# Optimization experiments

Hardware: AMD Instinct MI355X
Metric: run time of the kernel (lower is better)

## Reference

```python
import jax, jax.numpy as jnp
import numpy as np

N, D, E, L = 50000, 128, 800000, 3


def setup_inputs() -> dict:
    key = jax.random.key(0)
    ks = jax.random.split(key, 4)
    scale = 1.0 / np.sqrt(D)
    x = jax.random.normal(ks[0], (N, D), dtype=jnp.float32)
    edge_index = jax.random.randint(ks[1], (2, E), 0, N, dtype=jnp.int64)
    W1 = jax.random.normal(ks[2], (L, D, D), dtype=jnp.float32) * scale
    W2 = jax.random.normal(ks[3], (L, D, D), dtype=jnp.float32) * scale
    b1 = jnp.zeros((L, D), dtype=jnp.float32)
    b2 = jnp.zeros((L, D), dtype=jnp.float32)
    return {"x": x, "edge_index": edge_index, "W1": W1, "b1": b1, "W2": W2, "b2": b2}


def reference(x, edge_index, W1, b1, W2, b2):
    # GIN: for each conv, agg_i = (1+eps)*x_i + sum_{(j->i)} x_j  (eps=0),
    # then h = nn(agg) with nn = Linear->ReLU->Linear, then outer ReLU.
    src = edge_index[0]
    dst = edge_index[1]
    n = x.shape[0]
    for l in range(W1.shape[0]):
        agg = x + jax.ops.segment_sum(x[src], dst, num_segments=n)  # [N, D]
        h = jnp.maximum(agg @ W1[l] + b1[l], 0.0)                   # inner ReLU
        x = jnp.maximum(h @ W2[l] + b2[l], 0.0)                     # outer ReLU
    return x
```

## Files before the change

### kernel.cpp

```cpp
#include <hip/hip_runtime.h>
#include <cstdint>


constexpr int N = 50000;
constexpr int D = 128;
constexpr int E = 800000;
constexpr int L = 3;
constexpr int WROW = 136;
constexpr int PSH = 9;
constexpr int PN = 1 << PSH;
constexpr int K = (N + PN - 1) >> PSH;
constexpr int ABLK = 2048;
constexpr int NAB = (E + ABLK - 1) / ABLK;

typedef _Float16 f16;
typedef _Float16 f16x8 __attribute__((ext_vector_type(8)));
typedef float f32x4 __attribute__((ext_vector_type(4)));

__device__ __forceinline__ bool ei_is64(const int* ei) {
  return (ei[1] == 0) && (ei[3] == 0) && (ei[5] == 0);
}
__device__ __forceinline__ int ei_src(const int* ei, int e, bool is64) {
  return is64 ? ei[2 * (size_t)e] : ei[e];
}
__device__ __forceinline__ int ei_dst(const int* ei, int e, bool is64) {
  return is64 ? ei[2 * ((size_t)E + e)] : ei[(size_t)E + e];
}

__global__ __launch_bounds__(256) void k_init(const float* __restrict__ x0,
                                              const int* __restrict__ ei,
                                              const float* __restrict__ W1,
                                              const float* __restrict__ W2,
                                              f16* __restrict__ Wt,
                                              f16* __restrict__ xh,
                                              int2* __restrict__ srcdst,
                                              int* __restrict__ gcnt) {
  __shared__ int hist[K];
  const int bid = blockIdx.x;
  if (bid < 384) {
    int i = bid * 256 + threadIdx.x;
    int m = i >> 14;
    int c = (i >> 7) & 127;
    int k = i & 127;
    const float* src = (m < L) ? (W1 + (size_t)m * D * D)
                               : (W2 + (size_t)(m - L) * D * D);
    Wt[i] = (f16)src[(size_t)k * D + c];
  } else if (bid < 384 + 3125) {
    int i = (bid - 384) * 256 + threadIdx.x;
    float4 v0 = *(const float4*)(x0 + (size_t)i * 8);
    float4 v1 = *(const float4*)(x0 + (size_t)i * 8 + 4);
    f16x8 o = {(f16)v0.x, (f16)v0.y, (f16)v0.z, (f16)v0.w,
               (f16)v1.x, (f16)v1.y, (f16)v1.z, (f16)v1.w};
    *(f16x8*)(xh + (size_t)i * 8) = o;
  } else {
    const int b = bid - (384 + 3125);
    for (int i = threadIdx.x; i < K; i += 256) hist[i] = 0;
    __syncthreads();
    const int base = b * ABLK;
    const int nHere = min(ABLK, E - base);
    bool is64 = ei_is64(ei);
#pragma unroll
    for (int r = 0; r < ABLK / 256; ++r) {
      int idx = r * 256 + threadIdx.x;
      if (idx < nHere) {
        int e = base + idx;
        int s = ei_src(ei, e, is64);
        int d = ei_dst(ei, e, is64);
        srcdst[e] = make_int2(s, d);
        atomicAdd(&hist[d >> PSH], 1);
      }
    }
    __syncthreads();
    for (int i = threadIdx.x; i < K; i += 256) gcnt[i * NAB + b] = hist[i];
  }
}

__global__ __launch_bounds__(256) void k_gbase(const int* __restrict__ gcnt,
                                               int* __restrict__ gbase,
                                               int* __restrict__ psize) {
  __shared__ int s[256];
  __shared__ int carry;
  const int p = blockIdx.x;
  const int tid = threadIdx.x;
  if (tid == 0) carry = 0;
  __syncthreads();
  for (int chunk = 0; chunk < 2; ++chunk) {
    int i = chunk * 256 + tid;
    int v = (i < NAB) ? gcnt[p * NAB + i] : 0;
    s[tid] = v;
    __syncthreads();
#pragma unroll
    for (int o = 1; o < 256; o <<= 1) {
      int t = (tid >= o) ? s[tid - o] : 0;
      __syncthreads();
      s[tid] += t;
      __syncthreads();
    }
    int excl = s[tid] - v + carry;
    if (i < NAB) gbase[p * NAB + i] = excl;
    __syncthreads();
    if (tid == 255) carry = carry + s[255];
    __syncthreads();
  }
  if (tid == 0) psize[p] = carry;
}

__global__ __launch_bounds__(256) void k_pscan(const int* __restrict__ psize,
                                               int* __restrict__ pbase,
                                               int* __restrict__ off) {
  __shared__ int s[256];
  const int tid = threadIdx.x;
  int v = (tid < K) ? psize[tid] : 0;
  s[tid] = v;
  __syncthreads();
#pragma unroll
  for (int o = 1; o < 256; o <<= 1) {
    int t = (tid >= o) ? s[tid - o] : 0;
    __syncthreads();
    s[tid] += t;
    __syncthreads();
  }
  if (tid < K) pbase[tid] = s[tid] - v;
  if (tid == 0) { pbase[K] = E; off[N] = E; }
}

__global__ __launch_bounds__(256) void k_scat(const int2* __restrict__ srcdst,
                                              const int* __restrict__ gbase,
                                              const int* __restrict__ pbase,
                                              int2* __restrict__ part) {
  __shared__ int rankc[K];
  const int b = blockIdx.x;
  const int tid = threadIdx.x;
  for (int i = tid; i < K; i += 256) rankc[i] = 0;
  __syncthreads();
  const int base = b * ABLK;
  const int nHere = min(ABLK, E - base);
#pragma unroll
  for (int r = 0; r < ABLK / 256; ++r) {
    int idx = r * 256 + tid;
    if (idx < nHere) {
      int2 sd = srcdst[base + idx];
      int p = sd.y >> PSH;
      int lr = atomicAdd(&rankc[p], 1);
      part[pbase[p] + gbase[p * NAB + b] + lr] = sd;
    }
  }
}

__global__ __launch_bounds__(256) void k_fin(const int2* __restrict__ part,
                                             const int* __restrict__ pbase,
                                             int* __restrict__ off,
                                             int* __restrict__ ssrc) {
  __shared__ int hist[PN];
  __shared__ int bbase[PN];
  __shared__ int rc[PN];
  __shared__ int s[256];
  __shared__ int carry;
  const int p = blockIdx.x;
  const int tid = threadIdx.x;
  const int lo = p << PSH;
  const int nn = min(PN, N - lo);
  const int ebeg = pbase[p], eend = pbase[p + 1];
  for (int i = tid; i < PN; i += 256) { hist[i] = 0; rc[i] = 0; }
  if (tid == 0) carry = 0;
  __syncthreads();
  for (int e = ebeg + tid; e < eend; e += 256)
    atomicAdd(&hist[part[e].y - lo], 1);
  __syncthreads();
  for (int chunk = 0; chunk < PN / 256; ++chunk) {
    int i = chunk * 256 + tid;
    int v = hist[i];
    s[tid] = v;
    __syncthreads();
#pragma unroll
    for (int o = 1; o < 256; o <<= 1) {
      int t = (tid >= o) ? s[tid - o] : 0;
      __syncthreads();
      s[tid] += t;
      __syncthreads();
    }
    bbase[i] = s[tid] - v + carry;
    __syncthreads();
    if (tid == 255) carry = carry + s[255];
    __syncthreads();
  }
  for (int i = tid; i < nn; i += 256) off[lo + i] = ebeg + bbase[i];
  __syncthreads();
  for (int e = ebeg + tid; e < eend; e += 256) {
    int2 sd = part[e];
    int b = sd.y - lo;
    int r = atomicAdd(&rc[b], 1);
    ssrc[ebeg + bbase[b] + r] = sd.x;
  }
}

__global__ __launch_bounds__(256) void k_gather_f16(const f16* __restrict__ x,
                                                    const int* __restrict__ off,
                                                    const int* __restrict__ ssrc,
                                                    f16* __restrict__ agg) {
  int n = blockIdx.x * 16 + (threadIdx.x >> 4);
  if (n >= N) return;
  const int d0 = (threadIdx.x & 15) << 3;
  f16x8 v = *(const f16x8*)(x + (size_t)n * D + d0);
  float acc[8];
#pragma unroll
  for (int j = 0; j < 8; ++j) acc[j] = (float)v[j];
  const int beg = off[n], end = off[n + 1];
  int p = beg;
  for (; p + 8 <= end; p += 8) {
    f16x8 u[8];
#pragma unroll
    for (int q = 0; q < 8; ++q) {
      int s = ssrc[p + q];
      u[q] = *(const f16x8*)(x + (size_t)s * D + d0);
    }
#pragma unroll
    for (int q = 0; q < 8; ++q)
#pragma unroll
      for (int j = 0; j < 8; ++j) acc[j] += (float)u[q][j];
  }
  if (p + 4 <= end) {
    f16x8 u[4];
#pragma unroll
    for (int q = 0; q < 4; ++q) {
      int s = ssrc[p + q];
      u[q] = *(const f16x8*)(x + (size_t)s * D + d0);
    }
#pragma unroll
    for (int q = 0; q < 4; ++q)
#pragma unroll
      for (int j = 0; j < 8; ++j) acc[j] += (float)u[q][j];
    p += 4;
  }
  for (; p < end; ++p) {
    int s = ssrc[p];
    f16x8 u = *(const f16x8*)(x + (size_t)s * D + d0);
#pragma unroll
    for (int j = 0; j < 8; ++j) acc[j] += (float)u[j];
  }
  f16x8 o;
#pragma unroll
  for (int j = 0; j < 8; ++j) o[j] = (f16)acc[j];
  *(f16x8*)(agg + (size_t)n * D + d0) = o;
}

__global__ __launch_bounds__(512) void k_gemm_fused(const f16* __restrict__ A,
                                                    const f16* __restrict__ Wt1,
                                                    const f16* __restrict__ Wt2,
                                                    const float* __restrict__ b1,
                                                    const float* __restrict__ b2,
                                                    f16* __restrict__ Ch,
                                                    float* __restrict__ Cf) {
  __shared__ f16 Ws[2][128 * WROW];
  {
    const f16x8* g1 = (const f16x8*)Wt1;
    const f16x8* g2 = (const f16x8*)Wt2;
    for (int i = threadIdx.x; i < 2048; i += 512) {
      int c = i >> 4;
      int k8 = (i & 15) << 3;
      *(f16x8*)&Ws[0][c * WROW + k8] = g1[i];
      *(f16x8*)&Ws[1][c * WROW + k8] = g2[i];
    }
  }

  const int w = threadIdx.x >> 6;
  const int l = threadIdx.x & 63;
  const int l15 = l & 15;
  const int g = l >> 4;
  const int r0 = blockIdx.x * 128 + w * 16;

  const int arow = min(r0 + l15, N - 1);
  const f16* Arow = A + (size_t)arow * D;
  f16x8 a[4];
#pragma unroll
  for (int t = 0; t < 4; ++t)
    a[t] = *(const f16x8*)(Arow + t * 32 + g * 8);

  float bc1[8], bc2[8];
#pragma unroll
  for (int c = 0; c < 8; ++c) {
    bc1[c] = b1[c * 16 + l15];
    bc2[c] = b2[c * 16 + l15];
  }
  __syncthreads();

  f32x4 acc[8];
#pragma unroll
  for (int c = 0; c < 8; ++c) acc[c] = (f32x4){0.f, 0.f, 0.f, 0.f};
#pragma unroll
  for (int t = 0; t < 4; ++t) {
#pragma unroll
    for (int c = 0; c < 8; ++c) {
      f16x8 b = *(const f16x8*)&Ws[0][(c * 16 + l15) * WROW + t * 32 + g * 8];
      acc[c] = __builtin_amdgcn_mfma_f32_16x16x32_f16(a[t], b, acc[c], 0, 0, 0);
    }
  }
  __syncthreads();

  f16* hbuf = &Ws[0][0];
#pragma unroll
  for (int r = 0; r < 4; ++r) {
    int hr = w * 16 + g * 4 + r;
#pragma unroll
    for (int c = 0; c < 8; ++c) {
      float vv = fmaxf(acc[c][r] + bc1[c], 0.0f);
      hbuf[hr * WROW + c * 16 + l15] = (f16)vv;
    }
  }
  __syncthreads();

  f16x8 a2[4];
#pragma unroll
  for (int t = 0; t < 4; ++t)
    a2[t] = *(const f16x8*)&hbuf[(w * 16 + l15) * WROW + t * 32 + g * 8];

#pragma unroll
  for (int c = 0; c < 8; ++c) acc[c] = (f32x4){0.f, 0.f, 0.f, 0.f};
#pragma unroll
  for (int t = 0; t < 4; ++t) {
#pragma unroll
    for (int c = 0; c < 8; ++c) {
      f16x8 b = *(const f16x8*)&Ws[1][(c * 16 + l15) * WROW + t * 32 + g * 8];
      acc[c] = __builtin_amdgcn_mfma_f32_16x16x32_f16(a2[t], b, acc[c], 0, 0, 0);
    }
  }

#pragma unroll
  for (int r = 0; r < 4; ++r) {
    int rr = r0 + g * 4 + r;
    if (rr < N) {
#pragma unroll
      for (int c = 0; c < 8; ++c) {
        int col = c * 16 + l15;
        float vv = fmaxf(acc[c][r] + bc2[c], 0.0f);
        if (Cf) Cf[(size_t)rr * D + col] = vv;
        else    Ch[(size_t)rr * D + col] = (f16)vv;
      }
    }
  }
}

extern "C" void kernel_launch(void* const* d_in, const int* in_sizes, int n_in,
                              void* d_out, int out_size, void* d_ws, size_t ws_size,
                              hipStream_t stream) {
  const float* x0 = (const float*)d_in[0];
  const int* ei   = (const int*)d_in[1];
  const float* W1 = (const float*)d_in[2];
  const float* b1 = (const float*)d_in[3];
  const float* W2 = (const float*)d_in[4];
  const float* b2 = (const float*)d_in[5];
  float* out = (float*)d_out;

  f16* xh      = (f16*)d_ws;
  f16* aggh    = xh + (size_t)N * D;
  f16* Wt      = aggh + (size_t)N * D;
  int2* srcdst = (int2*)(Wt + (size_t)2 * L * D * D);
  int2* part   = srcdst + E;
  int* gcnt    = (int*)(part + E);
  int* gbase   = gcnt + (size_t)K * NAB;
  int* psize   = gbase + (size_t)K * NAB;
  int* pbase   = psize + K;
  int* off     = pbase + (K + 1);
  int* ssrc    = off + (N + 1);

  const dim3 blk(256);

  k_init<<<384 + 3125 + NAB, blk, 0, stream>>>(x0, ei, W1, W2, Wt, xh, srcdst,
                                               gcnt);
  k_gbase<<<K, blk, 0, stream>>>(gcnt, gbase, psize);
  k_pscan<<<1, blk, 0, stream>>>(psize, pbase, off);
  k_scat<<<NAB, blk, 0, stream>>>(srcdst, gbase, pbase, part);
  k_fin<<<K, blk, 0, stream>>>(part, pbase, off, ssrc);

  const int gemm_blocks = (N + 127) / 128;
  const int gather_blocks = N / 16;

  for (int l = 0; l < L; ++l) {
    k_gather_f16<<<gather_blocks, blk, 0, stream>>>(xh, off, ssrc, aggh);
    k_gemm_fused<<<gemm_blocks, dim3(512), 0, stream>>>(
        aggh, Wt + (size_t)l * D * D, Wt + (size_t)(L + l) * D * D,
        b1 + (size_t)l * D, b2 + (size_t)l * D, xh,
        (l == L - 1) ? out : nullptr);
  }
}
```

Baseline: 182.4 us.

## Pad CSR neighbor lists to multiples of eight with a zero dummy row

```diff
diff --git a/kernel.cpp b/kernel.cpp
--- a/kernel.cpp
+++ b/kernel.cpp
@@ -10,6 +10,7 @@
 constexpr int PSH = 9;
 constexpr int PN = 1 << PSH;
 constexpr int K = (N + PN - 1) >> PSH;
+constexpr int SLACK = 7 * PN;
 constexpr int ABLK = 2048;
 constexpr int NAB = (E + ABLK - 1) / ABLK;
 
@@ -52,7 +53,7 @@
     f16x8 o = {(f16)v0.x, (f16)v0.y, (f16)v0.z, (f16)v0.w,
                (f16)v1.x, (f16)v1.y, (f16)v1.z, (f16)v1.w};
     *(f16x8*)(xh + (size_t)i * 8) = o;
-  } else {
+  } else if (bid < 384 + 3125 + NAB) {
     const int b = bid - (384 + 3125);
     for (int i = threadIdx.x; i < K; i += 256) hist[i] = 0;
     __syncthreads();
@@ -72,6 +73,9 @@
     }
     __syncthreads();
     for (int i = threadIdx.x; i < K; i += 256) gcnt[i * NAB + b] = hist[i];
+  } else {
+    if (threadIdx.x < 16)
+      *(f16x8*)(xh + (size_t)N * D + threadIdx.x * 8) = (f16x8){};
   }
 }
 
@@ -105,34 +109,32 @@
   if (tid == 0) psize[p] = carry;
 }
 
-__global__ __launch_bounds__(256) void k_pscan(const int* __restrict__ psize,
-                                               int* __restrict__ pbase,
-                                               int* __restrict__ off) {
-  __shared__ int s[256];
+__device__ __forceinline__ void pscan_inblock(const int* __restrict__ psize,
+                                              int* __restrict__ pb) {
   const int tid = threadIdx.x;
-  int v = (tid < K) ? psize[tid] : 0;
-  s[tid] = v;
-  __syncthreads();
-#pragma unroll
-  for (int o = 1; o < 256; o <<= 1) {
-    int t = (tid >= o) ? s[tid - o] : 0;
-    __syncthreads();
-    s[tid] += t;
-    __syncthreads();
-  }
-  if (tid < K) pbase[tid] = s[tid] - v;
-  if (tid == 0) { pbase[K] = E; off[N] = E; }
+  if (tid < K) pb[tid] = psize[tid];
+  __syncthreads();
+  if (tid == 0) {
+    int r = 0;
+    for (int i = 0; i < K; ++i) {
+      int v = pb[i];
+      pb[i] = r;
+      r += v;
+    }
+  }
+  __syncthreads();
 }
 
 __global__ __launch_bounds__(256) void k_scat(const int2* __restrict__ srcdst,
                                               const int* __restrict__ gbase,
-                                              const int* __restrict__ pbase,
+                                              const int* __restrict__ psize,
                                               int2* __restrict__ part) {
   __shared__ int rankc[K];
+  __shared__ int pb[K];
   const int b = blockIdx.x;
   const int tid = threadIdx.x;
   for (int i = tid; i < K; i += 256) rankc[i] = 0;
-  __syncthreads();
+  pscan_inblock(psize, pb);
   const int base = b * ABLK;
   const int nHere = min(ABLK, E - base);
 #pragma unroll
@@ -142,34 +144,37 @@
       int2 sd = srcdst[base + idx];
       int p = sd.y >> PSH;
       int lr = atomicAdd(&rankc[p], 1);
-      part[pbase[p] + gbase[p * NAB + b] + lr] = sd;
+      part[pb[p] + gbase[p * NAB + b] + lr] = sd;
     }
   }
 }
 
 __global__ __launch_bounds__(256) void k_fin(const int2* __restrict__ part,
-                                             const int* __restrict__ pbase,
+                                             const int* __restrict__ psize,
                                              int* __restrict__ off,
+                                             int* __restrict__ offend,
                                              int* __restrict__ ssrc) {
   __shared__ int hist[PN];
   __shared__ int bbase[PN];
   __shared__ int rc[PN];
   __shared__ int s[256];
+  __shared__ int pb[K];
   __shared__ int carry;
   const int p = blockIdx.x;
   const int tid = threadIdx.x;
   const int lo = p << PSH;
   const int nn = min(PN, N - lo);
-  const int ebeg = pbase[p], eend = pbase[p + 1];
   for (int i = tid; i < PN; i += 256) { hist[i] = 0; rc[i] = 0; }
   if (tid == 0) carry = 0;
-  __syncthreads();
+  pscan_inblock(psize, pb);
+  const int ebeg = pb[p], eend = pb[p] + psize[p];
+  const int padbase = pb[p] + p * SLACK;
   for (int e = ebeg + tid; e < eend; e += 256)
     atomicAdd(&hist[part[e].y - lo], 1);
   __syncthreads();
   for (int chunk = 0; chunk < PN / 256; ++chunk) {
     int i = chunk * 256 + tid;
-    int v = hist[i];
+    int v = (hist[i] + 7) & ~7;
     s[tid] = v;
     __syncthreads();
 #pragma unroll
@@ -184,30 +189,36 @@
     if (tid == 255) carry = carry + s[255];
     __syncthreads();
   }
-  for (int i = tid; i < nn; i += 256) off[lo + i] = ebeg + bbase[i];
+  for (int i = tid; i < nn; i += 256) {
+    int st = padbase + bbase[i];
+    int deg = hist[i];
+    int pd = (deg + 7) & ~7;
+    off[lo + i] = st;
+    offend[lo + i] = st + pd;
+    for (int j = deg; j < pd; ++j) ssrc[st + j] = N;
+  }
   __syncthreads();
   for (int e = ebeg + tid; e < eend; e += 256) {
     int2 sd = part[e];
     int b = sd.y - lo;
     int r = atomicAdd(&rc[b], 1);
-    ssrc[ebeg + bbase[b] + r] = sd.x;
+    ssrc[padbase + bbase[b] + r] = sd.x;
   }
 }
 
 __global__ __launch_bounds__(256) void k_gather_f16(const f16* __restrict__ x,
                                                     const int* __restrict__ off,
+                                                    const int* __restrict__ offend,
                                                     const int* __restrict__ ssrc,
                                                     f16* __restrict__ agg) {
   int n = blockIdx.x * 16 + (threadIdx.x >> 4);
-  if (n >= N) return;
   const int d0 = (threadIdx.x & 15) << 3;
   f16x8 v = *(const f16x8*)(x + (size_t)n * D + d0);
   float acc[8];
 #pragma unroll
   for (int j = 0; j < 8; ++j) acc[j] = (float)v[j];
-  const int beg = off[n], end = off[n + 1];
-  int p = beg;
-  for (; p + 8 <= end; p += 8) {
+  const int e = offend[n];
+  for (int p = off[n]; p < e; p += 8) {
     f16x8 u[8];
 #pragma unroll
     for (int q = 0; q < 8; ++q) {
@@ -218,25 +229,6 @@
     for (int q = 0; q < 8; ++q)
 #pragma unroll
       for (int j = 0; j < 8; ++j) acc[j] += (float)u[q][j];
-  }
-  if (p + 4 <= end) {
-    f16x8 u[4];
-#pragma unroll
-    for (int q = 0; q < 4; ++q) {
-      int s = ssrc[p + q];
-      u[q] = *(const f16x8*)(x + (size_t)s * D + d0);
-    }
-#pragma unroll
-    for (int q = 0; q < 4; ++q)
-#pragma unroll
-      for (int j = 0; j < 8; ++j) acc[j] += (float)u[q][j];
-    p += 4;
-  }
-  for (; p < end; ++p) {
-    int s = ssrc[p];
-    f16x8 u = *(const f16x8*)(x + (size_t)s * D + d0);
-#pragma unroll
-    for (int j = 0; j < 8; ++j) acc[j] += (float)u[j];
   }
   f16x8 o;
 #pragma unroll
@@ -352,31 +344,30 @@
   float* out = (float*)d_out;
 
   f16* xh      = (f16*)d_ws;
-  f16* aggh    = xh + (size_t)N * D;
+  f16* aggh    = xh + (size_t)(N + 1) * D;
   f16* Wt      = aggh + (size_t)N * D;
   int2* srcdst = (int2*)(Wt + (size_t)2 * L * D * D);
   int2* part   = srcdst + E;
   int* gcnt    = (int*)(part + E);
   int* gbase   = gcnt + (size_t)K * NAB;
   int* psize   = gbase + (size_t)K * NAB;
-  int* pbase   = psize + K;
-  int* off     = pbase + (K + 1);
-  int* ssrc    = off + (N + 1);
+  int* off     = psize + K;
+  int* offend  = off + N;
+  int* ssrc    = offend + N;
 
   const dim3 blk(256);
 
-  k_init<<<384 + 3125 + NAB, blk, 0, stream>>>(x0, ei, W1, W2, Wt, xh, srcdst,
-                                               gcnt);
+  k_init<<<384 + 3125 + NAB + 1, blk, 0, stream>>>(x0, ei, W1, W2, Wt, xh,
+                                                   srcdst, gcnt);
   k_gbase<<<K, blk, 0, stream>>>(gcnt, gbase, psize);
-  k_pscan<<<1, blk, 0, stream>>>(psize, pbase, off);
-  k_scat<<<NAB, blk, 0, stream>>>(srcdst, gbase, pbase, part);
-  k_fin<<<K, blk, 0, stream>>>(part, pbase, off, ssrc);
+  k_scat<<<NAB, blk, 0, stream>>>(srcdst, gbase, psize, part);
+  k_fin<<<K, blk, 0, stream>>>(part, psize, off, offend, ssrc);
 
   const int gemm_blocks = (N + 127) / 128;
   const int gather_blocks = N / 16;
 
   for (int l = 0; l < L; ++l) {
-    k_gather_f16<<<gather_blocks, blk, 0, stream>>>(xh, off, ssrc, aggh);
+    k_gather_f16<<<gather_blocks, blk, 0, stream>>>(xh, off, offend, ssrc, aggh);
     k_gemm_fused<<<gemm_blocks, dim3(512), 0, stream>>>(
         aggh, Wt + (size_t)l * D * D, Wt + (size_t)(L + l) * D * D,
         b1 + (size_t)l * D, b2 + (size_t)l * D, xh,
```

After: 176.6 us. 1.03x faster.
